# Optimization experiments

Measured on AMD Instinct MI355X. Metric: run time of the kernel, lower is better.

## Reference

```python
import jax, jax.numpy as jnp
import numpy as np

MAX_SIZE = 650   # hard-coded node count in the original module
HIDDEN = 512     # hidden_dim
BATCH = 512      # batch_size (conv4 out channels)
IN_DIM = 512
N_EDGES = 150000


def _segment_softmax(e, dst, n):
    # torch_geometric.utils.softmax over destination-node segments
    m = jax.ops.segment_max(e, dst, num_segments=n)
    ex = jnp.exp(e - m[dst])
    s = jax.ops.segment_sum(ex, dst, num_segments=n)
    return ex / (s[dst] + 1e-16)


def _gat_conv(x, src, dst, W, a_src, a_dst, b, n, neg_slope=0.2):
    # PyG GATConv, heads=1, edge_dim=None (edge_attr ignored)
    h = x @ W                            # [n, out]
    al_s = h @ a_src                     # [n] per-node source attention logit
    al_d = h @ a_dst                     # [n] per-node dest attention logit
    e = jax.nn.leaky_relu(al_s[src] + al_d[dst], neg_slope)   # [E]
    alpha = _segment_softmax(e, dst, n)                        # [E]
    out = jax.ops.segment_sum(alpha[:, None] * h[src], dst, num_segments=n)
    return out + b


def setup_inputs() -> dict:
    key = jax.random.key(0)
    ks = jax.random.split(key, 12)
    inp = {
        "x_s": jax.random.normal(ks[0], (400, IN_DIM), jnp.float32),
        "x_t": jax.random.normal(ks[1], (250, IN_DIM), jnp.float32),
        "edge_index": jax.random.randint(ks[2], (2, N_EDGES), 0, MAX_SIZE, dtype=jnp.int32),
        "distances": jax.random.uniform(ks[3], (N_EDGES,), jnp.float32),
        "batch": jnp.zeros((MAX_SIZE,), jnp.int32),
        "W1": jax.random.normal(ks[4], (IN_DIM, HIDDEN), jnp.float32) / np.sqrt(IN_DIM).astype(np.float32),
        "a_src1": jax.random.normal(ks[5], (HIDDEN,), jnp.float32) * 0.1,
        "a_dst1": jax.random.normal(ks[6], (HIDDEN,), jnp.float32) * 0.1,
        "b1": jnp.zeros((HIDDEN,), jnp.float32),
        "W4": jax.random.normal(ks[7], (HIDDEN, BATCH), jnp.float32) / np.sqrt(HIDDEN).astype(np.float32),
        "a_src4": jax.random.normal(ks[8], (BATCH,), jnp.float32) * 0.1,
        "a_dst4": jax.random.normal(ks[9], (BATCH,), jnp.float32) * 0.1,
        "b4": jnp.zeros((BATCH,), jnp.float32),
        "fc_w": jax.random.normal(ks[10], (1, MAX_SIZE), jnp.float32) / np.sqrt(MAX_SIZE).astype(np.float32),
        "fc_b": jnp.zeros((1,), jnp.float32),
    }
    return inp


def reference(x_s, x_t, edge_index, distances, batch,
              W1, a_src1, a_dst1, b1, W4, a_src4, a_dst4, b4, fc_w, fc_b):
    # distances (edge_attr) and batch are unpacked but unused, as in the
    # original (GATConv with edge_dim=None ignores edge_attr).
    x = jnp.concatenate([x_s, x_t], axis=0)
    pad_n = max(MAX_SIZE - x.shape[0], 0)
    x = jnp.pad(x, ((0, pad_n), (0, 0)))            # [650, IN_DIM]
    # add_self_loops=True (PyG GATConv default)
    loop = jnp.arange(MAX_SIZE, dtype=edge_index.dtype)
    src = jnp.concatenate([edge_index[0], loop])
    dst = jnp.concatenate([edge_index[1], loop])
    x = _gat_conv(x, src, dst, W1, a_src1, a_dst1, b1, MAX_SIZE)
    x = jax.nn.relu(x)
    x = _gat_conv(x, src, dst, W4, a_src4, a_dst4, b4, MAX_SIZE)
    x = jax.nn.leaky_relu(x, 0.01)                  # [650, BATCH]
    x = x.reshape(BATCH, MAX_SIZE)                  # torch .view semantics (no transpose)
    x = x @ fc_w.T + fc_b                           # [BATCH, 1]
    x = x.squeeze()[None, :]                        # [1, BATCH]
    return jax.nn.sigmoid(x)
```

## Files before the change

kernel.cpp:

```cpp
#include <hip/hip_runtime.h>
#include <math.h>

#define N_NODES 650
#define DIM     512
#define E_RAW   150000
#define E_TOT   150650
#define NB      64
#define A_LD    704
#define S_H     (N_NODES * DIM)

__global__ __launch_bounds__(256)
void gemm4(const float* __restrict__ A0, const float* __restrict__ A1p,
           const float* __restrict__ abias, const float* __restrict__ B,
           float* __restrict__ P, int M, int lda, int Kb, int KC, int a_mode) {
    __shared__ float Ast[32][68];
    __shared__ float Bs[32][64];
    int t  = threadIdx.x;
    int tx = t & 15, ty = t >> 4;
    int row0 = blockIdx.y * 64, col0 = blockIdx.x * 64;
    int kbase = blockIdx.z * KC;
    float acc[4][4] = {};
    int m   = t >> 2;
    int kq  = (t & 3) * 4;
    int bkk = t >> 4;
    int bn4 = (t & 15) * 4;

    for (int kb = kbase; kb < kbase + KC; kb += 32) {
        float4 va = make_float4(0.f, 0.f, 0.f, 0.f);
        float4 vb = make_float4(0.f, 0.f, 0.f, 0.f);
        int gr = row0 + m;
        if (gr < M) {
            if (a_mode == 1) {
                const float* rp = (gr < 400) ? (A0 + (size_t)gr * 512)
                                             : (A1p + (size_t)(gr - 400) * 512);
                va = *(const float4*)(rp + kb + kq);
                vb = *(const float4*)(rp + kb + kq + 16);
            } else if (a_mode == 2) {
                size_t base = (size_t)gr * 512 + kb + kq;
                float4 p0 = *(const float4*)(A0 + base);
                float4 p1 = *(const float4*)(A1p + base);
                float4 bb = *(const float4*)(abias + kb + kq);
                va.x = p0.x + p1.x + bb.x; va.y = p0.y + p1.y + bb.y;
                va.z = p0.z + p1.z + bb.z; va.w = p0.w + p1.w + bb.w;
                p0 = *(const float4*)(A0 + base + 16);
                p1 = *(const float4*)(A1p + base + 16);
                bb = *(const float4*)(abias + kb + kq + 16);
                vb.x = p0.x + p1.x + bb.x; vb.y = p0.y + p1.y + bb.y;
                vb.z = p0.z + p1.z + bb.z; vb.w = p0.w + p1.w + bb.w;
                va.x = fmaxf(va.x, 0.f); va.y = fmaxf(va.y, 0.f);
                va.z = fmaxf(va.z, 0.f); va.w = fmaxf(va.w, 0.f);
                vb.x = fmaxf(vb.x, 0.f); vb.y = fmaxf(vb.y, 0.f);
                vb.z = fmaxf(vb.z, 0.f); vb.w = fmaxf(vb.w, 0.f);
            } else {
                const float* rp = A0 + (size_t)gr * lda;
                va = *(const float4*)(rp + kb + kq);
                vb = *(const float4*)(rp + kb + kq + 16);
            }
        }
        Ast[kq + 0][m] = va.x; Ast[kq + 1][m] = va.y;
        Ast[kq + 2][m] = va.z; Ast[kq + 3][m] = va.w;
        Ast[kq + 16][m] = vb.x; Ast[kq + 17][m] = vb.y;
        Ast[kq + 18][m] = vb.z; Ast[kq + 19][m] = vb.w;
        {
            int gk0 = kb + bkk, gk1 = gk0 + 16;
            float4 v0 = (gk0 < Kb) ? *(const float4*)&B[(size_t)gk0 * 512 + col0 + bn4]
                                   : make_float4(0.f, 0.f, 0.f, 0.f);
            float4 v1 = (gk1 < Kb) ? *(const float4*)&B[(size_t)gk1 * 512 + col0 + bn4]
                                   : make_float4(0.f, 0.f, 0.f, 0.f);
            *(float4*)&Bs[bkk][bn4]      = v0;
            *(float4*)&Bs[bkk + 16][bn4] = v1;
        }
        __syncthreads();
        #pragma unroll
        for (int kk = 0; kk < 32; kk++) {
            float4 av = *(const float4*)&Ast[kk][ty * 4];
            float4 bv = *(const float4*)&Bs[kk][tx * 4];
            acc[0][0] += av.x * bv.x; acc[0][1] += av.x * bv.y;
            acc[0][2] += av.x * bv.z; acc[0][3] += av.x * bv.w;
            acc[1][0] += av.y * bv.x; acc[1][1] += av.y * bv.y;
            acc[1][2] += av.y * bv.z; acc[1][3] += av.y * bv.w;
            acc[2][0] += av.z * bv.x; acc[2][1] += av.z * bv.y;
            acc[2][2] += av.z * bv.z; acc[2][3] += av.z * bv.w;
            acc[3][0] += av.w * bv.x; acc[3][1] += av.w * bv.y;
            acc[3][2] += av.w * bv.z; acc[3][3] += av.w * bv.w;
        }
        __syncthreads();
    }

    float* Pz = P + (size_t)blockIdx.z * S_H;
    #pragma unroll
    for (int i = 0; i < 4; i++) {
        int gr = row0 + ty * 4 + i;
        if (gr < M)
            *(float4*)&Pz[(size_t)gr * 512 + col0 + tx * 4] =
                make_float4(acc[i][0], acc[i][1], acc[i][2], acc[i][3]);
    }
}

__global__ __launch_bounds__(256)
void reduce_logits(const float* __restrict__ P,
                   const float* __restrict__ asrc, const float* __restrict__ adst,
                   float* __restrict__ h, float* __restrict__ als, float* __restrict__ ald) {
    __shared__ float red[8];
    int r = blockIdx.x, t = threadIdx.x;
    size_t base = (size_t)r * DIM;
    float v0 = P[base + t] + P[S_H + base + t];
    float v1 = P[base + t + 256] + P[S_H + base + t + 256];
    h[base + t]       = v0;
    h[base + t + 256] = v1;
    float ps = v0 * asrc[t] + v1 * asrc[t + 256];
    float pd = v0 * adst[t] + v1 * adst[t + 256];
    #pragma unroll
    for (int o = 32; o > 0; o >>= 1) {
        ps += __shfl_down(ps, o);
        pd += __shfl_down(pd, o);
    }
    if ((t & 63) == 0) { red[t >> 6] = ps; red[4 + (t >> 6)] = pd; }
    __syncthreads();
    if (t == 0) als[r] = red[0] + red[1] + red[2] + red[3];
    if (t == 1) ald[r] = red[4] + red[5] + red[6] + red[7];
}

__global__ __launch_bounds__(256)
void count_kernel(const int* __restrict__ ei, int* __restrict__ cntb) {
    __shared__ int h[N_NODES];
    for (int l = threadIdx.x; l < N_NODES; l += 256) h[l] = 0;
    __syncthreads();
    int per = (E_TOT + NB - 1) / NB;
    int e0 = blockIdx.x * per;
    int e1 = min(e0 + per, E_TOT);
    for (int i = e0 + threadIdx.x; i < e1; i += 256) {
        int d = (i < E_RAW) ? ei[E_RAW + i] : i - E_RAW;
        atomicAdd(&h[d], 1);
    }
    __syncthreads();
    for (int l = threadIdx.x; l < N_NODES; l += 256)
        cntb[blockIdx.x * N_NODES + l] = h[l];
}

__global__ __launch_bounds__(1024)
void scanbase_kernel(const int* __restrict__ cntb, int* __restrict__ rowptr,
                     int* __restrict__ baseb) {
    __shared__ int buf[1024];
    int t = threadIdx.x;
    int tot = 0;
    if (t < N_NODES)
        for (int b = 0; b < NB; b++) tot += cntb[b * N_NODES + t];
    buf[t] = (t < N_NODES) ? tot : 0;
    __syncthreads();
    #pragma unroll
    for (int o = 1; o < 1024; o <<= 1) {
        int v = (t >= o) ? buf[t - o] : 0;
        __syncthreads();
        buf[t] += v;
        __syncthreads();
    }
    if (t < N_NODES) {
        int run = buf[t] - tot;
        rowptr[t] = run;
        for (int b = 0; b < NB; b++) {
            baseb[b * N_NODES + t] = run;
            run += cntb[b * N_NODES + t];
        }
    }
    if (t == 0) rowptr[N_NODES] = E_TOT;
}

__global__ __launch_bounds__(256)
void scatter2_kernel(const int* __restrict__ ei, const int* __restrict__ baseb,
                     int* __restrict__ ssrc) {
    __shared__ int lcur[N_NODES];
    for (int l = threadIdx.x; l < N_NODES; l += 256)
        lcur[l] = baseb[blockIdx.x * N_NODES + l];
    __syncthreads();
    int per = (E_TOT + NB - 1) / NB;
    int e0 = blockIdx.x * per;
    int e1 = min(e0 + per, E_TOT);
    for (int i = e0 + threadIdx.x; i < e1; i += 256) {
        int s, d;
        if (i < E_RAW) { s = ei[i]; d = ei[E_RAW + i]; }
        else           { s = d = i - E_RAW; }
        int pos = atomicAdd(&lcur[d], 1);
        ssrc[pos] = s;
    }
}

__global__ __launch_bounds__(256)
void alpha_build(const int* __restrict__ rowptr, const int* __restrict__ ssrc,
                 const float* __restrict__ als, const float* __restrict__ ald,
                 float* __restrict__ Arow) {
    __shared__ float row[N_NODES];
    __shared__ float red[4];
    int d = blockIdx.x, t = threadIdx.x;
    for (int l = t; l < N_NODES; l += 256) row[l] = 0.f;
    __syncthreads();
    int r0 = rowptr[d], r1 = rowptr[d + 1];
    float aldd = ald[d];
    float psum = 0.f;
    for (int l = r0 + t; l < r1; l += 256) {
        int s = ssrc[l];
        float v = als[s] + aldd;
        v = v > 0.f ? v : 0.2f * v;
        float ex = __expf(v);
        atomicAdd(&row[s], ex);
        psum += ex;
    }
    #pragma unroll
    for (int o = 32; o > 0; o >>= 1) psum += __shfl_down(psum, o);
    if ((t & 63) == 0) red[t >> 6] = psum;
    __syncthreads();
    float inv = 1.f / (red[0] + red[1] + red[2] + red[3] + 1e-16f);
    for (int q = t; q < A_LD / 4; q += 256) {
        int c = q * 4;
        float4 v;
        v.x = (c + 0 < N_NODES) ? row[c + 0] * inv : 0.f;
        v.y = (c + 1 < N_NODES) ? row[c + 1] * inv : 0.f;
        v.z = (c + 2 < N_NODES) ? row[c + 2] * inv : 0.f;
        v.w = (c + 3 < N_NODES) ? row[c + 3] * inv : 0.f;
        *(float4*)&Arow[(size_t)d * A_LD + c] = v;
    }
}

__global__ void final_kernel(const float* __restrict__ Q,
                             const float* __restrict__ b4,
                             const float* __restrict__ fcw,
                             const float* __restrict__ fcb,
                             float* __restrict__ out) {
    int b = blockIdx.x * 4 + (threadIdx.x >> 6);
    int lane = threadIdx.x & 63;
    if (b >= 512) return;
    float s = 0.f;
    for (int i = lane; i < N_NODES; i += 64) {
        int g = b * N_NODES + i;
        float v = Q[g] + Q[S_H + g] + b4[g & 511];
        v = v > 0.f ? v : 0.01f * v;
        s += v * fcw[i];
    }
    #pragma unroll
    for (int o = 32; o > 0; o >>= 1) s += __shfl_down(s, o);
    if (lane == 0) out[b] = 1.f / (1.f + expf(-(s + fcb[0])));
}

extern "C" void kernel_launch(void* const* d_in, const int* in_sizes, int n_in,
                              void* d_out, int out_size, void* d_ws, size_t ws_size,
                              hipStream_t stream) {
    const float* x_s   = (const float*)d_in[0];
    const float* x_t   = (const float*)d_in[1];
    const int*   ei    = (const int*)d_in[2];
    const float* W1    = (const float*)d_in[5];
    const float* asrc1 = (const float*)d_in[6];
    const float* adst1 = (const float*)d_in[7];
    const float* b1    = (const float*)d_in[8];
    const float* W4    = (const float*)d_in[9];
    const float* asrc4 = (const float*)d_in[10];
    const float* adst4 = (const float*)d_in[11];
    const float* b4    = (const float*)d_in[12];
    const float* fcw   = (const float*)d_in[13];
    const float* fcb   = (const float*)d_in[14];
    float* out = (float*)d_out;

    float* ws = (float*)d_ws;
    int*   cntb   = (int*)ws;
    int*   baseb  = cntb + NB * N_NODES;
    int*   rowptr = baseb + NB * N_NODES;
    int*   ssrc   = rowptr + N_NODES + 1;
    float* als1   = (float*)(ssrc + E_TOT);
    float* ald1   = als1 + N_NODES;
    float* als2   = ald1 + N_NODES;
    float* ald2   = als2 + N_NODES;
    float* A1     = ald2 + N_NODES;
    float* A2     = A1 + (size_t)N_NODES * A_LD;
    float* P      = A2 + (size_t)N_NODES * A_LD;
    float* Q      = P + 2 * (size_t)S_H;
    float* h1     = Q + 2 * (size_t)S_H;
    float* h2     = h1 + (size_t)S_H;

    dim3 gG(8, 11, 2);

    count_kernel<<<NB, 256, 0, stream>>>(ei, cntb);
    scanbase_kernel<<<1, 1024, 0, stream>>>(cntb, rowptr, baseb);
    scatter2_kernel<<<NB, 256, 0, stream>>>(ei, baseb, ssrc);

    gemm4<<<gG, 256, 0, stream>>>(x_s, x_t, nullptr, W1, P, N_NODES, 512, 512, 256, 1);
    reduce_logits<<<N_NODES, 256, 0, stream>>>(P, asrc1, adst1, h1, als1, ald1);
    alpha_build<<<N_NODES, 256, 0, stream>>>(rowptr, ssrc, als1, ald1, A1);
    gemm4<<<gG, 256, 0, stream>>>(A1, nullptr, nullptr, h1, Q, N_NODES, A_LD, N_NODES, 352, 0);

    gemm4<<<gG, 256, 0, stream>>>(Q, Q + S_H, b1, W4, P, N_NODES, 512, 512, 256, 2);
    reduce_logits<<<N_NODES, 256, 0, stream>>>(P, asrc4, adst4, h2, als2, ald2);
    alpha_build<<<N_NODES, 256, 0, stream>>>(rowptr, ssrc, als2, ald2, A2);
    gemm4<<<gG, 256, 0, stream>>>(A2, nullptr, nullptr, h2, Q, N_NODES, A_LD, N_NODES, 352, 0);

    final_kernel<<<128, 256, 0, stream>>>(Q, b4, fcw, fcb, out);
}
```

Before: 201.2 us.

## Fuse all GAT stages into one persistent kernel with grid barriers

Replaces the dozen separate launches with a single persistent kernel of 512 blocks that walks through the stages and separates them with atomic-counter grid barriers. It raises the split-K factor from 2 to 4 and overlaps independent work inside one phase: CSR counting runs beside the first GEMM, and the layer-2 logits come from precomputed W4·a vectors so they run beside the second projection GEMM. This targets launch overhead and idle tail time between small kernels. In exchange, the spin-wait grid barriers depend on all 512 blocks being resident at once, and the extra split-K partials add memory traffic.

```diff
diff --git a/kernel.cpp b/kernel.cpp
--- a/kernel.cpp
+++ b/kernel.cpp
@@ -6,75 +6,93 @@
 #define E_RAW   150000
 #define E_TOT   150650
 #define NB      64
-#define A_LD    704
-#define S_H     (N_NODES * DIM)
-
-__global__ __launch_bounds__(256)
-void gemm4(const float* __restrict__ A0, const float* __restrict__ A1p,
-           const float* __restrict__ abias, const float* __restrict__ B,
-           float* __restrict__ P, int M, int lda, int Kb, int KC, int a_mode) {
-    __shared__ float Ast[32][68];
-    __shared__ float Bs[32][64];
+#define A_LD    768
+#define S_H     332800
+#define GRID    512
+
+__device__ __forceinline__ float4 ld4(const float* p) { return *(const float4*)p; }
+
+__device__ __forceinline__ void gsync(unsigned* gbar, unsigned target) {
+    __syncthreads();
+    if (threadIdx.x == 0) {
+        __threadfence();
+        atomicAdd(gbar, 1u);
+        volatile unsigned* vc = gbar;
+        while (*vc < target) { }
+    }
+    __syncthreads();
+    __threadfence();
+}
+
+__device__ __attribute__((noinline))
+void gemm_tile(int mode, const float* A0, const float* A1p,
+               const float* abias, const float* B, float* Pout,
+               int u, int KC, int KbB, int lda) {
+    __shared__ float SA[32 * 68];
+    __shared__ float SB[32 * 64];
     int t  = threadIdx.x;
     int tx = t & 15, ty = t >> 4;
-    int row0 = blockIdx.y * 64, col0 = blockIdx.x * 64;
-    int kbase = blockIdx.z * KC;
+    int col0 = (u & 7) * 64;
+    int row0 = ((u >> 3) % 11) * 64;
+    int z = u / 88;
+    int kbase = z * KC;
     float acc[4][4] = {};
-    int m   = t >> 2;
-    int kq  = (t & 3) * 4;
-    int bkk = t >> 4;
-    int bn4 = (t & 15) * 4;
+    int m = t >> 2, kq = (t & 3) * 4;
+    int bkk = t >> 4, bn4 = (t & 15) * 4;
 
     for (int kb = kbase; kb < kbase + KC; kb += 32) {
         float4 va = make_float4(0.f, 0.f, 0.f, 0.f);
-        float4 vb = make_float4(0.f, 0.f, 0.f, 0.f);
+        float4 vb = va;
         int gr = row0 + m;
-        if (gr < M) {
-            if (a_mode == 1) {
+        if (gr < N_NODES) {
+            if (mode == 1) {
                 const float* rp = (gr < 400) ? (A0 + (size_t)gr * 512)
                                              : (A1p + (size_t)(gr - 400) * 512);
-                va = *(const float4*)(rp + kb + kq);
-                vb = *(const float4*)(rp + kb + kq + 16);
-            } else if (a_mode == 2) {
+                va = ld4(rp + kb + kq);
+                vb = ld4(rp + kb + kq + 16);
+            } else if (mode == 2) {
                 size_t base = (size_t)gr * 512 + kb + kq;
-                float4 p0 = *(const float4*)(A0 + base);
-                float4 p1 = *(const float4*)(A1p + base);
-                float4 bb = *(const float4*)(abias + kb + kq);
-                va.x = p0.x + p1.x + bb.x; va.y = p0.y + p1.y + bb.y;
-                va.z = p0.z + p1.z + bb.z; va.w = p0.w + p1.w + bb.w;
-                p0 = *(const float4*)(A0 + base + 16);
-                p1 = *(const float4*)(A1p + base + 16);
-                bb = *(const float4*)(abias + kb + kq + 16);
-                vb.x = p0.x + p1.x + bb.x; vb.y = p0.y + p1.y + bb.y;
-                vb.z = p0.z + p1.z + bb.z; vb.w = p0.w + p1.w + bb.w;
-                va.x = fmaxf(va.x, 0.f); va.y = fmaxf(va.y, 0.f);
-                va.z = fmaxf(va.z, 0.f); va.w = fmaxf(va.w, 0.f);
-                vb.x = fmaxf(vb.x, 0.f); vb.y = fmaxf(vb.y, 0.f);
-                vb.z = fmaxf(vb.z, 0.f); vb.w = fmaxf(vb.w, 0.f);
+                float4 q0 = ld4(A0 + base);
+                float4 q1 = ld4(A0 + (size_t)S_H + base);
+                float4 q2 = ld4(A0 + 2 * (size_t)S_H + base);
+                float4 q3 = ld4(A0 + 3 * (size_t)S_H + base);
+                float4 bb = ld4(abias + kb + kq);
+                va.x = fmaxf(q0.x + q1.x + q2.x + q3.x + bb.x, 0.f);
+                va.y = fmaxf(q0.y + q1.y + q2.y + q3.y + bb.y, 0.f);
+                va.z = fmaxf(q0.z + q1.z + q2.z + q3.z + bb.z, 0.f);
+                va.w = fmaxf(q0.w + q1.w + q2.w + q3.w + bb.w, 0.f);
+                q0 = ld4(A0 + base + 16);
+                q1 = ld4(A0 + (size_t)S_H + base + 16);
+                q2 = ld4(A0 + 2 * (size_t)S_H + base + 16);
+                q3 = ld4(A0 + 3 * (size_t)S_H + base + 16);
+                bb = ld4(abias + kb + kq + 16);
+                vb.x = fmaxf(q0.x + q1.x + q2.x + q3.x + bb.x, 0.f);
+                vb.y = fmaxf(q0.y + q1.y + q2.y + q3.y + bb.y, 0.f);
+                vb.z = fmaxf(q0.z + q1.z + q2.z + q3.z + bb.z, 0.f);
+                vb.w = fmaxf(q0.w + q1.w + q2.w + q3.w + bb.w, 0.f);
             } else {
                 const float* rp = A0 + (size_t)gr * lda;
-                va = *(const float4*)(rp + kb + kq);
-                vb = *(const float4*)(rp + kb + kq + 16);
-            }
-        }
-        Ast[kq + 0][m] = va.x; Ast[kq + 1][m] = va.y;
-        Ast[kq + 2][m] = va.z; Ast[kq + 3][m] = va.w;
-        Ast[kq + 16][m] = vb.x; Ast[kq + 17][m] = vb.y;
-        Ast[kq + 18][m] = vb.z; Ast[kq + 19][m] = vb.w;
+                va = ld4(rp + kb + kq);
+                vb = ld4(rp + kb + kq + 16);
+            }
+        }
+        SA[(kq + 0) * 68 + m] = va.x; SA[(kq + 1) * 68 + m] = va.y;
+        SA[(kq + 2) * 68 + m] = va.z; SA[(kq + 3) * 68 + m] = va.w;
+        SA[(kq + 16) * 68 + m] = vb.x; SA[(kq + 17) * 68 + m] = vb.y;
+        SA[(kq + 18) * 68 + m] = vb.z; SA[(kq + 19) * 68 + m] = vb.w;
         {
             int gk0 = kb + bkk, gk1 = gk0 + 16;
-            float4 v0 = (gk0 < Kb) ? *(const float4*)&B[(size_t)gk0 * 512 + col0 + bn4]
-                                   : make_float4(0.f, 0.f, 0.f, 0.f);
-            float4 v1 = (gk1 < Kb) ? *(const float4*)&B[(size_t)gk1 * 512 + col0 + bn4]
-                                   : make_float4(0.f, 0.f, 0.f, 0.f);
-            *(float4*)&Bs[bkk][bn4]      = v0;
-            *(float4*)&Bs[bkk + 16][bn4] = v1;
+            float4 zf = make_float4(0.f, 0.f, 0.f, 0.f);
+            float4 v0 = (gk0 < KbB) ? ld4(&B[(size_t)gk0 * 512 + col0 + bn4]) : zf;
+            float4 v1 = (gk1 < KbB) ? ld4(&B[(size_t)gk1 * 512 + col0 + bn4]) : zf;
+            *(float4*)&SB[bkk * 64 + bn4] = v0;
+            *(float4*)&SB[(bkk + 16) * 64 + bn4] = v1;
         }
         __syncthreads();
         #pragma unroll
         for (int kk = 0; kk < 32; kk++) {
-            float4 av = *(const float4*)&Ast[kk][ty * 4];
-            float4 bv = *(const float4*)&Bs[kk][tx * 4];
+            float4 av = *(const float4*)&SA[kk * 68 + ty * 4];
+            float4 bv = *(const float4*)&SB[kk * 64 + tx * 4];
             acc[0][0] += av.x * bv.x; acc[0][1] += av.x * bv.y;
             acc[0][2] += av.x * bv.z; acc[0][3] += av.x * bv.w;
             acc[1][0] += av.y * bv.x; acc[1][1] += av.y * bv.y;
@@ -86,159 +104,283 @@
         }
         __syncthreads();
     }
-
-    float* Pz = P + (size_t)blockIdx.z * S_H;
+    float* Pz = Pout + (size_t)z * S_H;
     #pragma unroll
     for (int i = 0; i < 4; i++) {
         int gr = row0 + ty * 4 + i;
-        if (gr < M)
+        if (gr < N_NODES)
             *(float4*)&Pz[(size_t)gr * 512 + col0 + tx * 4] =
                 make_float4(acc[i][0], acc[i][1], acc[i][2], acc[i][3]);
     }
 }
 
-__global__ __launch_bounds__(256)
-void reduce_logits(const float* __restrict__ P,
-                   const float* __restrict__ asrc, const float* __restrict__ adst,
-                   float* __restrict__ h, float* __restrict__ als, float* __restrict__ ald) {
-    __shared__ float red[8];
-    int r = blockIdx.x, t = threadIdx.x;
-    size_t base = (size_t)r * DIM;
-    float v0 = P[base + t] + P[S_H + base + t];
-    float v1 = P[base + t + 256] + P[S_H + base + t + 256];
-    h[base + t]       = v0;
-    h[base + t + 256] = v1;
-    float ps = v0 * asrc[t] + v1 * asrc[t + 256];
-    float pd = v0 * adst[t] + v1 * adst[t + 256];
-    #pragma unroll
-    for (int o = 32; o > 0; o >>= 1) {
-        ps += __shfl_down(ps, o);
-        pd += __shfl_down(pd, o);
-    }
-    if ((t & 63) == 0) { red[t >> 6] = ps; red[4 + (t >> 6)] = pd; }
-    __syncthreads();
-    if (t == 0) als[r] = red[0] + red[1] + red[2] + red[3];
-    if (t == 1) ald[r] = red[4] + red[5] + red[6] + red[7];
-}
-
-__global__ __launch_bounds__(256)
-void count_kernel(const int* __restrict__ ei, int* __restrict__ cntb) {
-    __shared__ int h[N_NODES];
-    for (int l = threadIdx.x; l < N_NODES; l += 256) h[l] = 0;
-    __syncthreads();
-    int per = (E_TOT + NB - 1) / NB;
-    int e0 = blockIdx.x * per;
-    int e1 = min(e0 + per, E_TOT);
-    for (int i = e0 + threadIdx.x; i < e1; i += 256) {
-        int d = (i < E_RAW) ? ei[E_RAW + i] : i - E_RAW;
-        atomicAdd(&h[d], 1);
-    }
-    __syncthreads();
-    for (int l = threadIdx.x; l < N_NODES; l += 256)
-        cntb[blockIdx.x * N_NODES + l] = h[l];
-}
-
-__global__ __launch_bounds__(1024)
-void scanbase_kernel(const int* __restrict__ cntb, int* __restrict__ rowptr,
-                     int* __restrict__ baseb) {
-    __shared__ int buf[1024];
+__global__ __launch_bounds__(256, 2)
+void mega(const float* __restrict__ x_s, const float* __restrict__ x_t,
+          const int* __restrict__ ei,
+          const float* __restrict__ W1, const float* __restrict__ asrc1,
+          const float* __restrict__ adst1, const float* __restrict__ b1,
+          const float* __restrict__ W4, const float* __restrict__ asrc4,
+          const float* __restrict__ adst4, const float* __restrict__ b4,
+          const float* __restrict__ fcw, const float* __restrict__ fcb,
+          float* __restrict__ out, void* wsraw) {
+    unsigned* gbar = (unsigned*)wsraw;
+    float* fp = (float*)wsraw + 4;
+    float* P    = fp;  fp += 4 * (size_t)S_H;
+    float* Q    = fp;  fp += 4 * (size_t)S_H;
+    float* h1   = fp;  fp += S_H;
+    float* h2   = fp;  fp += S_H;
+    float* A1   = fp;  fp += (size_t)N_NODES * A_LD;
+    float* A2   = fp;  fp += (size_t)N_NODES * A_LD;
+    int* ip     = (int*)fp;
+    int* ssrc   = ip;  ip += E_TOT;
+    int* cntN   = ip;  ip += N_NODES * NB;
+    int* baseb  = ip;  ip += N_NODES * NB;
+    int* rowptr = ip;  ip += N_NODES + 1;
+    float* als1 = (float*)ip;
+    float* ald1 = als1 + N_NODES;
+    float* als2 = ald1 + N_NODES;
+    float* ald2 = als2 + N_NODES;
+    float* ws2v = ald2 + N_NODES;
+    float* wd2v = ws2v + 512;
+
+    __shared__ int   iLC[N_NODES];
+    __shared__ float fA[A_LD];
+    __shared__ float redf[8];
     int t = threadIdx.x;
-    int tot = 0;
-    if (t < N_NODES)
-        for (int b = 0; b < NB; b++) tot += cntb[b * N_NODES + t];
-    buf[t] = (t < N_NODES) ? tot : 0;
-    __syncthreads();
-    #pragma unroll
-    for (int o = 1; o < 1024; o <<= 1) {
-        int v = (t >= o) ? buf[t - o] : 0;
-        __syncthreads();
-        buf[t] += v;
-        __syncthreads();
-    }
-    if (t < N_NODES) {
-        int run = buf[t] - tot;
-        rowptr[t] = run;
-        for (int b = 0; b < NB; b++) {
-            baseb[b * N_NODES + t] = run;
-            run += cntb[b * N_NODES + t];
-        }
-    }
-    if (t == 0) rowptr[N_NODES] = E_TOT;
-}
-
-__global__ __launch_bounds__(256)
-void scatter2_kernel(const int* __restrict__ ei, const int* __restrict__ baseb,
-                     int* __restrict__ ssrc) {
-    __shared__ int lcur[N_NODES];
-    for (int l = threadIdx.x; l < N_NODES; l += 256)
-        lcur[l] = baseb[blockIdx.x * N_NODES + l];
-    __syncthreads();
-    int per = (E_TOT + NB - 1) / NB;
-    int e0 = blockIdx.x * per;
-    int e1 = min(e0 + per, E_TOT);
-    for (int i = e0 + threadIdx.x; i < e1; i += 256) {
-        int s, d;
-        if (i < E_RAW) { s = ei[i]; d = ei[E_RAW + i]; }
-        else           { s = d = i - E_RAW; }
-        int pos = atomicAdd(&lcur[d], 1);
-        ssrc[pos] = s;
-    }
-}
-
-__global__ __launch_bounds__(256)
-void alpha_build(const int* __restrict__ rowptr, const int* __restrict__ ssrc,
-                 const float* __restrict__ als, const float* __restrict__ ald,
-                 float* __restrict__ Arow) {
-    __shared__ float row[N_NODES];
-    __shared__ float red[4];
-    int d = blockIdx.x, t = threadIdx.x;
-    for (int l = t; l < N_NODES; l += 256) row[l] = 0.f;
-    __syncthreads();
-    int r0 = rowptr[d], r1 = rowptr[d + 1];
-    float aldd = ald[d];
-    float psum = 0.f;
-    for (int l = r0 + t; l < r1; l += 256) {
-        int s = ssrc[l];
-        float v = als[s] + aldd;
-        v = v > 0.f ? v : 0.2f * v;
-        float ex = __expf(v);
-        atomicAdd(&row[s], ex);
-        psum += ex;
-    }
-    #pragma unroll
-    for (int o = 32; o > 0; o >>= 1) psum += __shfl_down(psum, o);
-    if ((t & 63) == 0) red[t >> 6] = psum;
-    __syncthreads();
-    float inv = 1.f / (red[0] + red[1] + red[2] + red[3] + 1e-16f);
-    for (int q = t; q < A_LD / 4; q += 256) {
-        int c = q * 4;
-        float4 v;
-        v.x = (c + 0 < N_NODES) ? row[c + 0] * inv : 0.f;
-        v.y = (c + 1 < N_NODES) ? row[c + 1] * inv : 0.f;
-        v.z = (c + 2 < N_NODES) ? row[c + 2] * inv : 0.f;
-        v.w = (c + 3 < N_NODES) ? row[c + 3] * inv : 0.f;
-        *(float4*)&Arow[(size_t)d * A_LD + c] = v;
-    }
-}
-
-__global__ void final_kernel(const float* __restrict__ Q,
-                             const float* __restrict__ b4,
-                             const float* __restrict__ fcw,
-                             const float* __restrict__ fcb,
-                             float* __restrict__ out) {
-    int b = blockIdx.x * 4 + (threadIdx.x >> 6);
-    int lane = threadIdx.x & 63;
-    if (b >= 512) return;
-    float s = 0.f;
-    for (int i = lane; i < N_NODES; i += 64) {
-        int g = b * N_NODES + i;
-        float v = Q[g] + Q[S_H + g] + b4[g & 511];
-        v = v > 0.f ? v : 0.01f * v;
-        s += v * fcw[i];
-    }
-    #pragma unroll
-    for (int o = 32; o > 0; o >>= 1) s += __shfl_down(s, o);
-    if (lane == 0) out[b] = 1.f / (1.f + expf(-(s + fcb[0])));
+    int lane = t & 63, wv = t >> 6;
+    const int per = (E_TOT + NB - 1) / NB;
+    unsigned bar = 0;
+
+    for (int u = blockIdx.x; u < 432; u += gridDim.x) {
+        if (u < 352) {
+            gemm_tile(1, x_s, x_t, nullptr, W1, P, u, 128, 512, 512);
+        } else if (u < 416) {
+            int cu = u - 352;
+            __syncthreads();
+            for (int n = t; n < N_NODES; n += 256) iLC[n] = 0;
+            __syncthreads();
+            int e0 = cu * per, e1 = min(e0 + per, E_TOT);
+            for (int i = e0 + t; i < e1; i += 256) {
+                int d = (i < E_RAW) ? ei[E_RAW + i] : i - E_RAW;
+                atomicAdd(&iLC[d], 1);
+            }
+            __syncthreads();
+            for (int n = t; n < N_NODES; n += 256) cntN[n * NB + cu] = iLC[n];
+        } else {
+            int mu = u - 416;
+            const float* av = (mu >> 3) ? adst4 : asrc4;
+            float* outv = (mu >> 3) ? wd2v : ws2v;
+            int rg = mu & 7;
+            for (int rr = 0; rr < 16; rr++) {
+                int r = rg * 64 + rr * 4 + wv;
+                float s = 0.f;
+                for (int c = lane; c < 512; c += 64) s += W4[(size_t)r * 512 + c] * av[c];
+                #pragma unroll
+                for (int o = 32; o > 0; o >>= 1) s += __shfl_down(s, o);
+                if (lane == 0) outv[r] = s;
+            }
+        }
+    }
+    bar += GRID; gsync(gbar, bar);
+
+    for (int u = blockIdx.x; u < 651; u += gridDim.x) {
+        __syncthreads();
+        if (u < 650) {
+            int r = u;
+            size_t base = (size_t)r * 512;
+            float v0 = P[base + t] + P[S_H + base + t] +
+                       P[2 * (size_t)S_H + base + t] + P[3 * (size_t)S_H + base + t];
+            float v1 = P[base + t + 256] + P[S_H + base + t + 256] +
+                       P[2 * (size_t)S_H + base + t + 256] + P[3 * (size_t)S_H + base + t + 256];
+            h1[base + t] = v0;
+            h1[base + t + 256] = v1;
+            float ps = v0 * asrc1[t] + v1 * asrc1[t + 256];
+            float pd = v0 * adst1[t] + v1 * adst1[t + 256];
+            #pragma unroll
+            for (int o = 32; o > 0; o >>= 1) {
+                ps += __shfl_down(ps, o);
+                pd += __shfl_down(pd, o);
+            }
+            if (lane == 0) { redf[wv] = ps; redf[4 + wv] = pd; }
+            __syncthreads();
+            if (t == 0) als1[r] = redf[0] + redf[1] + redf[2] + redf[3];
+            if (t == 1) ald1[r] = redf[4] + redf[5] + redf[6] + redf[7];
+        } else {
+            int n0 = 3 * t;
+            int tv[3]; int chunk = 0;
+            #pragma unroll
+            for (int j = 0; j < 3; j++) {
+                int n = n0 + j; int s = 0;
+                if (n < N_NODES) {
+                    for (int b = 0; b < NB; b += 4) {
+                        int4 c4 = *(const int4*)&cntN[n * NB + b];
+                        s += c4.x + c4.y + c4.z + c4.w;
+                    }
+                }
+                tv[j] = s; chunk += s;
+            }
+            iLC[t] = chunk;
+            __syncthreads();
+            for (int o = 1; o < 256; o <<= 1) {
+                int x = (t >= o) ? iLC[t - o] : 0;
+                __syncthreads();
+                iLC[t] += x;
+                __syncthreads();
+            }
+            int run = iLC[t] - chunk;
+            #pragma unroll
+            for (int j = 0; j < 3; j++) {
+                int n = n0 + j;
+                if (n < N_NODES) {
+                    rowptr[n] = run;
+                    for (int b = 0; b < NB; b++) {
+                        baseb[n * NB + b] = run;
+                        run += cntN[n * NB + b];
+                    }
+                }
+            }
+            if (t == 0) rowptr[N_NODES] = E_TOT;
+        }
+    }
+    bar += GRID; gsync(gbar, bar);
+
+    for (int u = blockIdx.x; u < NB; u += gridDim.x) {
+        __syncthreads();
+        for (int n = t; n < N_NODES; n += 256) iLC[n] = baseb[n * NB + u];
+        __syncthreads();
+        int e0 = u * per, e1 = min(e0 + per, E_TOT);
+        for (int i = e0 + t; i < e1; i += 256) {
+            int s, d;
+            if (i < E_RAW) { s = ei[i]; d = ei[E_RAW + i]; }
+            else           { s = d = i - E_RAW; }
+            int pos = atomicAdd(&iLC[d], 1);
+            ssrc[pos] = s;
+        }
+    }
+    bar += GRID; gsync(gbar, bar);
+
+    for (int u = blockIdx.x; u < N_NODES; u += gridDim.x) {
+        __syncthreads();
+        for (int l = t; l < A_LD; l += 256) fA[l] = 0.f;
+        __syncthreads();
+        int r0 = rowptr[u], r1 = rowptr[u + 1];
+        float aldd = ald1[u];
+        float psum = 0.f;
+        for (int l = r0 + t; l < r1; l += 256) {
+            int s = ssrc[l];
+            float v = als1[s] + aldd;
+            v = v > 0.f ? v : 0.2f * v;
+            float ex = __expf(v);
+            atomicAdd(&fA[s], ex);
+            psum += ex;
+        }
+        #pragma unroll
+        for (int o = 32; o > 0; o >>= 1) psum += __shfl_down(psum, o);
+        if (lane == 0) redf[wv] = psum;
+        __syncthreads();
+        float inv = 1.f / (redf[0] + redf[1] + redf[2] + redf[3] + 1e-16f);
+        for (int q = t; q < A_LD / 4; q += 256) {
+            float4 v = *(const float4*)&fA[q * 4];
+            v.x *= inv; v.y *= inv; v.z *= inv; v.w *= inv;
+            *(float4*)&A1[(size_t)u * A_LD + q * 4] = v;
+        }
+    }
+    bar += GRID; gsync(gbar, bar);
+
+    for (int u = blockIdx.x; u < 352; u += gridDim.x)
+        gemm_tile(0, A1, nullptr, nullptr, h1, Q, u, 192, N_NODES, A_LD);
+    bar += GRID; gsync(gbar, bar);
+
+    for (int u = blockIdx.x; u < 1002; u += gridDim.x) {
+        if (u < 352) {
+            gemm_tile(2, Q, nullptr, b1, W4, P, u, 128, 512, 512);
+        } else {
+            int r = u - 352;
+            __syncthreads();
+            size_t base = (size_t)r * 512;
+            float ps = 0.f, pd = 0.f;
+            for (int k = t; k < 512; k += 256) {
+                float v = Q[base + k] + Q[S_H + base + k] +
+                          Q[2 * (size_t)S_H + base + k] + Q[3 * (size_t)S_H + base + k] + b1[k];
+                v = fmaxf(v, 0.f);
+                ps += v * ws2v[k];
+                pd += v * wd2v[k];
+            }
+            #pragma unroll
+            for (int o = 32; o > 0; o >>= 1) {
+                ps += __shfl_down(ps, o);
+                pd += __shfl_down(pd, o);
+            }
+            if (lane == 0) { redf[wv] = ps; redf[4 + wv] = pd; }
+            __syncthreads();
+            if (t == 0) als2[r] = redf[0] + redf[1] + redf[2] + redf[3];
+            if (t == 1) ald2[r] = redf[4] + redf[5] + redf[6] + redf[7];
+        }
+    }
+    bar += GRID; gsync(gbar, bar);
+
+    for (int u = blockIdx.x; u < 1300; u += gridDim.x) {
+        __syncthreads();
+        if (u < 650) {
+            size_t base = (size_t)u * 512;
+            float v0 = P[base + t] + P[S_H + base + t] +
+                       P[2 * (size_t)S_H + base + t] + P[3 * (size_t)S_H + base + t];
+            float v1 = P[base + t + 256] + P[S_H + base + t + 256] +
+                       P[2 * (size_t)S_H + base + t + 256] + P[3 * (size_t)S_H + base + t + 256];
+            h2[base + t] = v0;
+            h2[base + t + 256] = v1;
+        } else {
+            int d = u - 650;
+            for (int l = t; l < A_LD; l += 256) fA[l] = 0.f;
+            __syncthreads();
+            int r0 = rowptr[d], r1 = rowptr[d + 1];
+            float aldd = ald2[d];
+            float psum = 0.f;
+            for (int l = r0 + t; l < r1; l += 256) {
+                int s = ssrc[l];
+                float v = als2[s] + aldd;
+                v = v > 0.f ? v : 0.2f * v;
+                float ex = __expf(v);
+                atomicAdd(&fA[s], ex);
+                psum += ex;
+            }
+            #pragma unroll
+            for (int o = 32; o > 0; o >>= 1) psum += __shfl_down(psum, o);
+            if (lane == 0) redf[wv] = psum;
+            __syncthreads();
+            float inv = 1.f / (redf[0] + redf[1] + redf[2] + redf[3] + 1e-16f);
+            for (int q = t; q < A_LD / 4; q += 256) {
+                float4 v = *(const float4*)&fA[q * 4];
+                v.x *= inv; v.y *= inv; v.z *= inv; v.w *= inv;
+                *(float4*)&A2[(size_t)d * A_LD + q * 4] = v;
+            }
+        }
+    }
+    bar += GRID; gsync(gbar, bar);
+
+    for (int u = blockIdx.x; u < 352; u += gridDim.x)
+        gemm_tile(0, A2, nullptr, nullptr, h2, Q, u, 192, N_NODES, A_LD);
+    bar += GRID; gsync(gbar, bar);
+
+    for (int u = blockIdx.x; u < 512; u += gridDim.x) {
+        __syncthreads();
+        float s = 0.f;
+        for (int i = t; i < N_NODES; i += 256) {
+            int g = u * N_NODES + i;
+            float v = Q[g] + Q[S_H + g] + Q[2 * (size_t)S_H + g] +
+                      Q[3 * (size_t)S_H + g] + b4[g & 511];
+            v = v > 0.f ? v : 0.01f * v;
+            s += v * fcw[i];
+        }
+        #pragma unroll
+        for (int o = 32; o > 0; o >>= 1) s += __shfl_down(s, o);
+        if (lane == 0) redf[wv] = s;
+        __syncthreads();
+        if (t == 0) {
+            float tot = redf[0] + redf[1] + redf[2] + redf[3];
+            out[u] = 1.f / (1.f + expf(-(tot + fcb[0])));
+        }
+    }
 }
 
 extern "C" void kernel_launch(void* const* d_in, const int* in_sizes, int n_in,
@@ -259,37 +401,9 @@
     const float* fcb   = (const float*)d_in[14];
     float* out = (float*)d_out;
 
-    float* ws = (float*)d_ws;
-    int*   cntb   = (int*)ws;
-    int*   baseb  = cntb + NB * N_NODES;
-    int*   rowptr = baseb + NB * N_NODES;
-    int*   ssrc   = rowptr + N_NODES + 1;
-    float* als1   = (float*)(ssrc + E_TOT);
-    float* ald1   = als1 + N_NODES;
-    float* als2   = ald1 + N_NODES;
-    float* ald2   = als2 + N_NODES;
-    float* A1     = ald2 + N_NODES;
-    float* A2     = A1 + (size_t)N_NODES * A_LD;
-    float* P      = A2 + (size_t)N_NODES * A_LD;
-    float* Q      = P + 2 * (size_t)S_H;
-    float* h1     = Q + 2 * (size_t)S_H;
-    float* h2     = h1 + (size_t)S_H;
-
-    dim3 gG(8, 11, 2);
-
-    count_kernel<<<NB, 256, 0, stream>>>(ei, cntb);
-    scanbase_kernel<<<1, 1024, 0, stream>>>(cntb, rowptr, baseb);
-    scatter2_kernel<<<NB, 256, 0, stream>>>(ei, baseb, ssrc);
-
-    gemm4<<<gG, 256, 0, stream>>>(x_s, x_t, nullptr, W1, P, N_NODES, 512, 512, 256, 1);
-    reduce_logits<<<N_NODES, 256, 0, stream>>>(P, asrc1, adst1, h1, als1, ald1);
-    alpha_build<<<N_NODES, 256, 0, stream>>>(rowptr, ssrc, als1, ald1, A1);
-    gemm4<<<gG, 256, 0, stream>>>(A1, nullptr, nullptr, h1, Q, N_NODES, A_LD, N_NODES, 352, 0);
-
-    gemm4<<<gG, 256, 0, stream>>>(Q, Q + S_H, b1, W4, P, N_NODES, 512, 512, 256, 2);
-    reduce_logits<<<N_NODES, 256, 0, stream>>>(P, asrc4, adst4, h2, als2, ald2);
-    alpha_build<<<N_NODES, 256, 0, stream>>>(rowptr, ssrc, als2, ald2, A2);
-    gemm4<<<gG, 256, 0, stream>>>(A2, nullptr, nullptr, h2, Q, N_NODES, A_LD, N_NODES, 352, 0);
-
-    final_kernel<<<128, 256, 0, stream>>>(Q, b4, fcw, fcb, out);
+    hipMemsetAsync(d_ws, 0, 16, stream);
+
+    mega<<<dim3(GRID), dim3(256), 0, stream>>>(
+        x_s, x_t, ei, W1, asrc1, adst1, b1,
+        W4, asrc4, adst4, b4, fcw, fcb, out, d_ws);
 }
```

Result: slower. 774.0 us (+284.8%).
